# Kernel optimization log

Hardware: AMD Instinct MI355X
Metric: run time of the kernel (lower is better)

Reference implementation:

```python
import jax, jax.numpy as jnp
import numpy as np

HIDDEN = 256
NUM_CLASSES = 25
INPUT_DIM = 76


def _lstm_layer(x, Wi, Wh, b):
    """Flax OptimizedLSTMCell semantics: gates [i, f, g, o], zero-init carry.
    x: [B, T, D]; Wi: [D, 4H]; Wh: [H, 4H]; b: [4H]. Returns hidden seq [B, T, H]."""
    B = x.shape[0]
    H = Wh.shape[0]
    c0 = jnp.zeros((B, H), x.dtype)
    h0 = jnp.zeros((B, H), x.dtype)

    def step(carry, xt):
        c, h = carry
        z = xt @ Wi + h @ Wh + b  # [B, 4H]
        i, f, g, o = jnp.split(z, 4, axis=-1)
        i = jax.nn.sigmoid(i)
        f = jax.nn.sigmoid(f)
        g = jnp.tanh(g)
        o = jax.nn.sigmoid(o)
        c = f * c + i * g
        h = o * jnp.tanh(c)
        return (c, h), h

    (_, _), ys = jax.lax.scan(step, (c0, h0), jnp.swapaxes(x, 0, 1))  # scan over time
    return jnp.swapaxes(ys, 0, 1)  # [B, T, H]


def setup_inputs() -> dict:
    key = jax.random.key(0)
    ks = jax.random.split(key, 9)
    B, T, D, H = 512, 512, INPUT_DIM, HIDDEN
    s_in = 1.0 / np.sqrt(D)
    s_h = 1.0 / np.sqrt(H)
    return {
        "x": jax.random.normal(ks[0], (B, T, D), jnp.float32),
        "Wi1": jax.random.normal(ks[1], (D, 4 * H), jnp.float32) * s_in,
        "Wh1": jax.random.normal(ks[2], (H, 4 * H), jnp.float32) * s_h,
        "b1": jnp.zeros((4 * H,), jnp.float32),
        "Wi2": jax.random.normal(ks[3], (H, 4 * H), jnp.float32) * s_h,
        "Wh2": jax.random.normal(ks[4], (H, 4 * H), jnp.float32) * s_h,
        "b2": jnp.zeros((4 * H,), jnp.float32),
        "Wd": jax.random.normal(ks[5], (H, NUM_CLASSES), jnp.float32) * s_h,
        "bd": jnp.zeros((NUM_CLASSES,), jnp.float32),
    }


def reference(x, Wi1, Wh1, b1, Wi2, Wh2, b2, Wd, bd):
    h1 = _lstm_layer(x, Wi1, Wh1, b1)   # [B, T, H]
    h2 = _lstm_layer(h1, Wi2, Wh2, b2)  # [B, T, H]
    feats = h2[:, -1]                   # dropout deterministic (eval mode)
    logits = feats @ Wd + bd            # [B, num_classes]
    return logits
```

## Files before the change

kernel.cpp:

```cpp
#include <hip/hip_runtime.h>

#define BB 512
#define TT 512
#define DD 76
#define HH 256
#define NC 25
#define NBLK 256
#define NTHREADS 512
#define BBHH (BB * HH)

#define K1 352
#define K2 512
#define WS1 360
#define WS2 520

typedef unsigned short u16;
typedef unsigned int u32;
typedef unsigned long long u64;
typedef __attribute__((ext_vector_type(8))) short bf16x8;
typedef __attribute__((ext_vector_type(4))) float f32x4;

__device__ __forceinline__ float bf2f(u16 v) {
  union { u32 u; float f; } c; c.u = ((u32)v) << 16; return c.f;
}
__device__ __forceinline__ u16 f2bf(float f) {
  union { u32 u; float f; } c; c.f = f;
  u32 r = c.u + 0x7FFFu + ((c.u >> 16) & 1u);
  return (u16)(r >> 16);
}
__device__ __forceinline__ void split2(float f, u16& h, u16& l) {
  u16 hh = f2bf(f);
  float r = f - bf2f(hh);
  h = hh; l = f2bf(r);
}
__device__ __forceinline__ float tanh_f(float v) {
  float e = __expf(2.0f * v);
  return 1.0f - 2.0f / (e + 1.0f);
}
__device__ __forceinline__ float gact(float v, bool is_tanh) {
  float e = __expf(is_tanh ? 2.0f * v : -v);
  float inv = 1.0f / (1.0f + e);
  return is_tanh ? 1.0f - 2.0f * inv : inv;
}

__device__ __forceinline__ u64 ald2(const u32* p) {
  return __hip_atomic_load((const u64*)p, __ATOMIC_RELAXED, __HIP_MEMORY_SCOPE_AGENT);
}
__device__ __forceinline__ u32 ald1(const u32* p) {
  return __hip_atomic_load(p, __ATOMIC_RELAXED, __HIP_MEMORY_SCOPE_AGENT);
}
__device__ __forceinline__ void ast1(u32* p, u32 v) {
  __hip_atomic_store(p, v, __ATOMIC_RELAXED, __HIP_MEMORY_SCOPE_AGENT);
}

__device__ __forceinline__ void wait_flags(const u32* fbase, u32 target) {
  const int tid = threadIdx.x;
  if (tid < 32) {
    const u32* p = fbase + tid * 32;
    while (__hip_atomic_load(p, __ATOMIC_RELAXED, __HIP_MEMORY_SCOPE_AGENT) < target)
      __builtin_amdgcn_s_sleep(1);
  }
  __syncthreads();
}
__device__ __forceinline__ void post_flag(u32* slot, u32 val) {
  __syncthreads();
  if (threadIdx.x == 0) ast1(slot, val);
}

__device__ __forceinline__ bf16x8 hi8(const u64 w[4]) {
  union { u32 u[4]; bf16x8 v; } c;
#pragma unroll
  for (int i = 0; i < 4; ++i)
    c.u[i] = __builtin_amdgcn_perm((u32)(w[i] >> 32), (u32)w[i], 0x05040100u);
  return c.v;
}
__device__ __forceinline__ bf16x8 lo8(const u64 w[4]) {
  union { u32 u[4]; bf16x8 v; } c;
#pragma unroll
  for (int i = 0; i < 4; ++i)
    c.u[i] = __builtin_amdgcn_perm((u32)(w[i] >> 32), (u32)w[i], 0x07060302u);
  return c.v;
}

__device__ __forceinline__ void splitv8(const float* f, bf16x8& vh, bf16x8& vl) {
  union { u16 s[8]; bf16x8 v; } ch, cl;
#pragma unroll
  for (int i = 0; i < 8; ++i) { u16 h_, l_; split2(f[i], h_, l_); ch.s[i] = h_; cl.s[i] = l_; }
  vh = ch.v; vl = cl.v;
}

__global__ void repack_kernel(const float* __restrict__ Wi1, const float* __restrict__ Wh1,
                              const float* __restrict__ Wi2, const float* __restrict__ Wh2,
                              u16* __restrict__ w1hg, u16* __restrict__ w1lg,
                              u16* __restrict__ w2hg, u16* __restrict__ w2lg) {
  int idx = blockIdx.x * blockDim.x + threadIdx.x;
  const int N1 = 1024 * K1;
  if (idx < N1) {
    int c = idx / K1, k = idx - c * K1;
    int src = (c & 3) * HH + (c >> 2);
    float v = 0.f;
    if (k < HH) v = Wh1[k * 1024 + src];
    else if (k < HH + DD) v = Wi1[(k - HH) * 1024 + src];
    u16 h, l; split2(v, h, l);
    w1hg[idx] = h; w1lg[idx] = l;
  } else if (idx < N1 + 1024 * K2) {
    int d = idx - N1;
    int c = d >> 9, k = d & 511;
    int src = (c & 3) * HH + (c >> 2);
    float v = (k < HH) ? Wi2[k * 1024 + src] : Wh2[(k - HH) * 1024 + src];
    u16 h, l; split2(v, h, l);
    w2hg[d] = h; w2lg[d] = l;
  }
}

#define MFMA3(AA, AB, AC, AH, AL, BH, BL)                                   \
  { (AA) = __builtin_amdgcn_mfma_f32_16x16x32_bf16(AH, BH, (AA), 0, 0, 0);  \
    (AB) = __builtin_amdgcn_mfma_f32_16x16x32_bf16(AH, BL, (AB), 0, 0, 0);  \
    (AC) = __builtin_amdgcn_mfma_f32_16x16x32_bf16(AL, BH, (AC), 0, 0, 0); }

#define MFMA_CH(AH, AL, PH0, PL0, PH1, PL1, KOFF)                           \
  { bf16x8 b0h_ = *(const bf16x8*)((PH0) + (KOFF));                         \
    bf16x8 b0l_ = *(const bf16x8*)((PL0) + (KOFF));                         \
    bf16x8 b1h_ = *(const bf16x8*)((PH1) + (KOFF));                         \
    bf16x8 b1l_ = *(const bf16x8*)((PL1) + (KOFF));                         \
    MFMA3(aA0, aB0, aC0, AH, AL, b0h_, b0l_)                                \
    MFMA3(aA1, aB1, aC1, AH, AL, b1h_, b1l_) }

#define GATES(Z, CS, DW)                                                    \
  _Pragma("unroll")                                                         \
  for (int r = 0; r < 4; ++r) {                                             \
    float a_ = gact((Z)[r], gi == 2);                                       \
    float v1_ = __shfl_xor(a_, 1);                                          \
    float v2_ = __shfl_xor(a_, 2);                                          \
    float v3_ = __shfl_xor(a_, 3);                                          \
    float cn_ = v1_ * (CS)[r] + a_ * v2_;                                   \
    (CS)[r] = cn_;                                                          \
    float hv_ = v3_ * tanh_f(cn_);                                          \
    if (gi == 0) {                                                          \
      u16 hh_, hl_; split2(hv_, hh_, hl_);                                  \
      ast1((DW) + (size_t)(rbase + r) * HH + jg, (u32)hh_ | ((u32)hl_ << 16)); \
    }                                                                       \
  }

__global__ __launch_bounds__(NTHREADS, 2) void lstm_kernel(
    const float* __restrict__ x,
    const float* __restrict__ b1, const float* __restrict__ b2,
    const float* __restrict__ Wd, const float* __restrict__ bd,
    const u16* __restrict__ w1hg, const u16* __restrict__ w1lg,
    const u16* __restrict__ w2hg, const u16* __restrict__ w2lg,
    u32* __restrict__ h1w, u32* __restrict__ h2w,
    u32* __restrict__ flags,
    float* __restrict__ out)
{
  __shared__ u16 w1h[32 * WS1], w1l[32 * WS1];
  __shared__ u16 w2h[32 * WS2], w2l[32 * WS2];
  __shared__ float zx[2][8][64][4];

  const int tid = threadIdx.x;
  const int lane = tid & 63;
  const int wv = tid >> 6;
  const int m  = wv & 3;
  const int kh = wv >> 2;
  const int nl = lane & 15;
  const int qd = lane >> 4;
  const int bt = blockIdx.x & 7;
  const int jt = blockIdx.x >> 3;
  const int row0 = bt * 64;

  u32* gAp = flags + bt * 1024;
  u32* gBp = flags + 8192 + bt * 1024;
  u32* gAslot = gAp + jt * 32;
  u32* gBslot = gBp + jt * 32;

  for (int i = tid; i < 32 * (K1 / 2); i += NTHREADS) {
    int c = i / 176, kk = i - c * 176;
    ((u32*)&w1h[c * WS1])[kk] = ((const u32*)(w1hg + (size_t)(jt * 32 + c) * K1))[kk];
    ((u32*)&w1l[c * WS1])[kk] = ((const u32*)(w1lg + (size_t)(jt * 32 + c) * K1))[kk];
  }
  for (int i = tid; i < 32 * (K2 / 2); i += NTHREADS) {
    int c = i >> 8, kk = i & 255;
    ((u32*)&w2h[c * WS2])[kk] = ((const u32*)(w2hg + (size_t)(jt * 32 + c) * K2))[kk];
    ((u32*)&w2l[c * WS2])[kk] = ((const u32*)(w2lg + (size_t)(jt * 32 + c) * K2))[kk];
  }

  const int cg_col = jt * 32 + kh * 16 + nl;
  const int jg = cg_col >> 2;
  const int gi = cg_col & 3;
  const int rbase = row0 + m * 16 + qd * 4;

  float ab1[2], ab2[2];
#pragma unroll
  for (int tl = 0; tl < 2; ++tl) {
    int col = jt * 32 + tl * 16 + nl;
    float v1 = b1[(col & 3) * HH + (col >> 2)];
    float v2 = b2[(col & 3) * HH + (col >> 2)];
    ab1[tl] = (kh == 0) ? v1 : 0.f;
    ab2[tl] = (kh == 0) ? v2 : 0.f;
  }

  const int arow = row0 + m * 16 + nl;

  const u16* pB1h0 = w1h + nl * WS1;
  const u16* pB1l0 = w1l + nl * WS1;
  const u16* pB1h1 = w1h + (16 + nl) * WS1;
  const u16* pB1l1 = w1l + (16 + nl) * WS1;
  const u16* pB2h0 = w2h + nl * WS2;
  const u16* pB2l0 = w2l + nl * WS2;
  const u16* pB2h1 = w2h + (16 + nl) * WS2;
  const u16* pB2l1 = w2l + (16 + nl) * WS2;

  float cs1[4] = {0.f, 0.f, 0.f, 0.f}, cs2[4] = {0.f, 0.f, 0.f, 0.f};
  bf16x8 h1fh[4], h1fl[4];

  __syncthreads();

  {
    f32x4 aA0 = {ab1[0], ab1[0], ab1[0], ab1[0]};
    f32x4 aA1 = {ab1[1], ab1[1], ab1[1], ab1[1]};
    f32x4 aB0 = {0,0,0,0}, aB1 = {0,0,0,0}, aC0 = {0,0,0,0}, aC1 = {0,0,0,0};
    const float* xrow = x + (size_t)arow * TT * DD;
    if (kh == 0) {
#pragma unroll
      for (int ci = 0; ci < 2; ++ci) {
        float xv[8];
        float4 f0 = *(const float4*)(xrow + ci * 32 + qd * 8);
        float4 f1 = *(const float4*)(xrow + ci * 32 + qd * 8 + 4);
        xv[0]=f0.x; xv[1]=f0.y; xv[2]=f0.z; xv[3]=f0.w;
        xv[4]=f1.x; xv[5]=f1.y; xv[6]=f1.z; xv[7]=f1.w;
        bf16x8 xh, xl; splitv8(xv, xh, xl);
        const int koff = (8 + ci) * 32 + qd * 8;
        MFMA_CH(xh, xl, pB1h0, pB1l0, pB1h1, pB1l1, koff)
      }
    } else {
      float xv[8] = {0,0,0,0,0,0,0,0};
      if (qd == 0) {
        float4 f0 = *(const float4*)(xrow + 64);
        float4 f1 = *(const float4*)(xrow + 68);
        xv[0]=f0.x; xv[1]=f0.y; xv[2]=f0.z; xv[3]=f0.w;
        xv[4]=f1.x; xv[5]=f1.y; xv[6]=f1.z; xv[7]=f1.w;
      } else if (qd == 1) {
        float4 f0 = *(const float4*)(xrow + 72);
        xv[0]=f0.x; xv[1]=f0.y; xv[2]=f0.z; xv[3]=f0.w;
      }
      bf16x8 xh, xl; splitv8(xv, xh, xl);
      const int koff = 10 * 32 + qd * 8;
      MFMA_CH(xh, xl, pB1h0, pB1l0, pB1h1, pB1l1, koff)
    }
    f32x4 zk = (kh == 0) ? (aA0 + aB0 + aC0) : (aA1 + aB1 + aC1);
    f32x4 zo = (kh == 0) ? (aA1 + aB1 + aC1) : (aA0 + aB0 + aC0);
    *(f32x4*)&zx[1][wv][lane][0] = zo;
    __syncthreads();
    zk += *(const f32x4*)&zx[1][wv ^ 4][lane][0];
    GATES(zk, cs1, h1w)
    __syncthreads();
    if (tid == 0) { ast1(gAslot, 1u); ast1(gBslot, 1u); }
  }

#pragma unroll 1
  for (int t = 0; t < TT; ++t) {
    const u32* h1cw = h1w + (t & 1) * BBHH;
    u32* h1nw = h1w + ((t + 1) & 1) * BBHH;
    const u32* h2pw = h2w + ((t + 1) & 1) * BBHH;
    u32* h2cw = h2w + (t & 1) * BBHH;

    {
      f32x4 aA0 = {ab2[0], ab2[0], ab2[0], ab2[0]};
      f32x4 aA1 = {ab2[1], ab2[1], ab2[1], ab2[1]};
      f32x4 aB0 = {0,0,0,0}, aB1 = {0,0,0,0}, aC0 = {0,0,0,0}, aC1 = {0,0,0,0};

      wait_flags(gAp, t + 1);
      u64 rw2[4][4];
      if (t > 0) {
        const u32* hp = h2pw + (size_t)arow * HH + kh * 128;
#pragma unroll
        for (int i = 0; i < 4; ++i) {
          const u32* p = hp + i * 32 + qd * 8;
          rw2[i][0] = ald2(p);     rw2[i][1] = ald2(p + 2);
          rw2[i][2] = ald2(p + 4); rw2[i][3] = ald2(p + 6);
        }
      }
      wait_flags(gBp, t + 1);
      u64 rw1[4][4];
      {
        const u32* hp = h1cw + (size_t)arow * HH + kh * 128;
#pragma unroll
        for (int i = 0; i < 4; ++i) {
          const u32* p = hp + i * 32 + qd * 8;
          rw1[i][0] = ald2(p);     rw1[i][1] = ald2(p + 2);
          rw1[i][2] = ald2(p + 4); rw1[i][3] = ald2(p + 6);
        }
      }
      if (t > 0) {
#pragma unroll
        for (int i = 0; i < 4; ++i) {
          bf16x8 ah = hi8(rw2[i]), al = lo8(rw2[i]);
          const int koff = (8 + kh * 4 + i) * 32 + qd * 8;
          MFMA_CH(ah, al, pB2h0, pB2l0, pB2h1, pB2l1, koff)
        }
      }
#pragma unroll
      for (int i = 0; i < 4; ++i) {
        h1fh[i] = hi8(rw1[i]); h1fl[i] = lo8(rw1[i]);
        const int koff = (kh * 4 + i) * 32 + qd * 8;
        MFMA_CH(h1fh[i], h1fl[i], pB2h0, pB2l0, pB2h1, pB2l1, koff)
      }
      f32x4 zk = (kh == 0) ? (aA0 + aB0 + aC0) : (aA1 + aB1 + aC1);
      f32x4 zo = (kh == 0) ? (aA1 + aB1 + aC1) : (aA0 + aB0 + aC0);
      *(f32x4*)&zx[0][wv][lane][0] = zo;
      __syncthreads();
      zk += *(const f32x4*)&zx[0][wv ^ 4][lane][0];
      GATES(zk, cs2, h2cw)
      post_flag(gAslot, t + 2);
    }

    if (t < TT - 1) {
      f32x4 aA0 = {ab1[0], ab1[0], ab1[0], ab1[0]};
      f32x4 aA1 = {ab1[1], ab1[1], ab1[1], ab1[1]};
      f32x4 aB0 = {0,0,0,0}, aB1 = {0,0,0,0}, aC0 = {0,0,0,0}, aC1 = {0,0,0,0};
      const float* xrow = x + ((size_t)arow * TT + (t + 1)) * DD;

      if (kh == 0) {
#pragma unroll
        for (int ci = 0; ci < 2; ++ci) {
          float xv[8];
          float4 f0 = *(const float4*)(xrow + ci * 32 + qd * 8);
          float4 f1 = *(const float4*)(xrow + ci * 32 + qd * 8 + 4);
          xv[0]=f0.x; xv[1]=f0.y; xv[2]=f0.z; xv[3]=f0.w;
          xv[4]=f1.x; xv[5]=f1.y; xv[6]=f1.z; xv[7]=f1.w;
          bf16x8 xh, xl; splitv8(xv, xh, xl);
          const int koff = (8 + ci) * 32 + qd * 8;
          MFMA_CH(xh, xl, pB1h0, pB1l0, pB1h1, pB1l1, koff)
        }
      } else {
        float xv[8] = {0,0,0,0,0,0,0,0};
        if (qd == 0) {
          float4 f0 = *(const float4*)(xrow + 64);
          float4 f1 = *(const float4*)(xrow + 68);
          xv[0]=f0.x; xv[1]=f0.y; xv[2]=f0.z; xv[3]=f0.w;
          xv[4]=f1.x; xv[5]=f1.y; xv[6]=f1.z; xv[7]=f1.w;
        } else if (qd == 1) {
          float4 f0 = *(const float4*)(xrow + 72);
          xv[0]=f0.x; xv[1]=f0.y; xv[2]=f0.z; xv[3]=f0.w;
        }
        bf16x8 xh, xl; splitv8(xv, xh, xl);
        const int koff = 10 * 32 + qd * 8;
        MFMA_CH(xh, xl, pB1h0, pB1l0, pB1h1, pB1l1, koff)
      }
#pragma unroll
      for (int i = 0; i < 4; ++i) {
        const int koff = (kh * 4 + i) * 32 + qd * 8;
        MFMA_CH(h1fh[i], h1fl[i], pB1h0, pB1l0, pB1h1, pB1l1, koff)
      }
      f32x4 zk = (kh == 0) ? (aA0 + aB0 + aC0) : (aA1 + aB1 + aC1);
      f32x4 zo = (kh == 0) ? (aA1 + aB1 + aC1) : (aA0 + aB0 + aC0);
      *(f32x4*)&zx[1][wv][lane][0] = zo;
      __syncthreads();
      zk += *(const f32x4*)&zx[1][wv ^ 4][lane][0];
      GATES(zk, cs1, h1nw)
      post_flag(gBslot, t + 2);
    }
  }

  wait_flags(gAp, TT + 1);
  if (tid < 2 * NC) {
    int r = row0 + jt * 2 + tid / NC;
    int n = tid - (tid / NC) * NC;
    float s = bd[n];
    const u32* fw = h2w + BBHH + (size_t)r * HH;
#pragma unroll 8
    for (int k = 0; k < HH; ++k) {
      u32 w = ald1(fw + k);
      s += (bf2f((u16)w) + bf2f((u16)(w >> 16))) * Wd[k * NC + n];
    }
    out[r * NC + n] = s;
  }
}

extern "C" void kernel_launch(void* const* d_in, const int* in_sizes, int n_in,
                              void* d_out, int out_size, void* d_ws, size_t ws_size,
                              hipStream_t stream) {
  const float* x   = (const float*)d_in[0];
  const float* Wi1 = (const float*)d_in[1];
  const float* Wh1 = (const float*)d_in[2];
  const float* b1  = (const float*)d_in[3];
  const float* Wi2 = (const float*)d_in[4];
  const float* Wh2 = (const float*)d_in[5];
  const float* b2  = (const float*)d_in[6];
  const float* Wd  = (const float*)d_in[7];
  const float* bd  = (const float*)d_in[8];

  char* ws = (char*)d_ws;
  u32* h1w = (u32*)(ws);
  u32* h2w = (u32*)(ws + 1048576u);
  u16* w1hg = (u16*)(ws + 2097152u);
  u16* w1lg = (u16*)(ws + 2097152u + 720896u);
  u16* w2hg = (u16*)(ws + 2097152u + 2u * 720896u);
  u16* w2lg = (u16*)(ws + 2097152u + 2u * 720896u + 1048576u);
  u32* flags = (u32*)(ws + 5636096u);
  float* out = (float*)d_out;

  hipMemsetAsync((void*)flags, 0, 65536, stream);
  const int total = 1024 * K1 + 1024 * K2;
  repack_kernel<<<(total + 255) / 256, 256, 0, stream>>>(
      Wi1, Wh1, Wi2, Wh2, w1hg, w1lg, w2hg, w2lg);

  void* args[] = {
    (void*)&x, (void*)&b1, (void*)&b2, (void*)&Wd, (void*)&bd,
    (void*)&w1hg, (void*)&w1lg, (void*)&w2hg, (void*)&w2lg,
    (void*)&h1w, (void*)&h2w,
    (void*)&flags, (void*)&out
  };
  (void)hipLaunchCooperativeKernel((void*)lstm_kernel, dim3(NBLK),
                                   dim3(NTHREADS), args, 0, stream);
}
```

Measured before the change: 5.749 ms.

## Reorder layer-1 step ahead of layer-2 and coalesce hidden-state stores

Each timestep now computes the layer-1 update for t+1 first, using h1 values prefetched in the previous iteration. The layer-2 step then runs, and the wait and load of the next h1 is placed inside it, so the cross-block flag wait overlaps with layer-2 MFMA work. Hidden-state writes are gathered across lanes with shuffles and issued as two 64-bit stores per row from one lane, instead of scattered 32-bit stores from a quarter of the lanes. The x loads are hoisted ahead of the recurrent MFMAs to hide their latency. The cost is extra register pressure from the prefetched h1 buffer and a reworked synchronization order that must still be correct.

```diff
diff --git a/kernel.cpp b/kernel.cpp
--- a/kernel.cpp
+++ b/kernel.cpp
@@ -50,6 +50,9 @@
   return __hip_atomic_load(p, __ATOMIC_RELAXED, __HIP_MEMORY_SCOPE_AGENT);
 }
 __device__ __forceinline__ void ast1(u32* p, u32 v) {
+  __hip_atomic_store(p, v, __ATOMIC_RELAXED, __HIP_MEMORY_SCOPE_AGENT);
+}
+__device__ __forceinline__ void ast2(u64* p, u64 v) {
   __hip_atomic_store(p, v, __ATOMIC_RELAXED, __HIP_MEMORY_SCOPE_AGENT);
 }
 
@@ -126,21 +129,42 @@
     MFMA3(aA0, aB0, aC0, AH, AL, b0h_, b0l_)                                \
     MFMA3(aA1, aB1, aC1, AH, AL, b1h_, b1l_) }
 
-#define GATES(Z, CS, DW)                                                    \
-  _Pragma("unroll")                                                         \
-  for (int r = 0; r < 4; ++r) {                                             \
-    float a_ = gact((Z)[r], gi == 2);                                       \
-    float v1_ = __shfl_xor(a_, 1);                                          \
-    float v2_ = __shfl_xor(a_, 2);                                          \
-    float v3_ = __shfl_xor(a_, 3);                                          \
-    float cn_ = v1_ * (CS)[r] + a_ * v2_;                                   \
-    (CS)[r] = cn_;                                                          \
-    float hv_ = v3_ * tanh_f(cn_);                                          \
-    if (gi == 0) {                                                          \
+#define GATES_ST(Z, CS, DST)                                                \
+  { u32 hwv[4];                                                             \
+    _Pragma("unroll")                                                       \
+    for (int r = 0; r < 4; ++r) {                                           \
+      float a_ = gact((Z)[r], gi == 2);                                     \
+      float v1_ = __shfl_xor(a_, 1);                                        \
+      float v2_ = __shfl_xor(a_, 2);                                        \
+      float v3_ = __shfl_xor(a_, 3);                                        \
+      float cn_ = v1_ * (CS)[r] + a_ * v2_;                                 \
+      (CS)[r] = cn_;                                                        \
+      float hv_ = v3_ * tanh_f(cn_);                                        \
       u16 hh_, hl_; split2(hv_, hh_, hl_);                                  \
-      ast1((DW) + (size_t)(rbase + r) * HH + jg, (u32)hh_ | ((u32)hl_ << 16)); \
+      hwv[r] = (u32)hh_ | ((u32)hl_ << 16);                                 \
     }                                                                       \
-  }
+    _Pragma("unroll")                                                       \
+    for (int r = 0; r < 4; ++r) {                                           \
+      int base_ = lane & 48;                                                \
+      u32 w1_ = __shfl(hwv[r], base_ + 4);                                  \
+      u32 w2_ = __shfl(hwv[r], base_ + 8);                                  \
+      u32 w3_ = __shfl(hwv[r], base_ + 12);                                 \
+      if (nl == 0) {                                                        \
+        u64* dp_ = (u64*)((DST) + (size_t)(rbase + r) * HH + jt * 8 + kh * 4); \
+        ast2(dp_,     (u64)hwv[r] | ((u64)w1_ << 32));                      \
+        ast2(dp_ + 1, (u64)w2_    | ((u64)w3_ << 32));                      \
+      }                                                                     \
+    }                                                                       \
+  }
+
+#define LOAD_RW(RW, BASEPTR)                                                \
+  { const u32* hp_ = (BASEPTR) + (size_t)arow * HH + kh * 128;              \
+    _Pragma("unroll")                                                       \
+    for (int i_ = 0; i_ < 4; ++i_) {                                        \
+      const u32* p_ = hp_ + i_ * 32 + qd * 8;                               \
+      (RW)[i_][0] = ald2(p_);     (RW)[i_][1] = ald2(p_ + 2);               \
+      (RW)[i_][2] = ald2(p_ + 4); (RW)[i_][3] = ald2(p_ + 6);               \
+    } }
 
 __global__ __launch_bounds__(NTHREADS, 2) void lstm_kernel(
     const float* __restrict__ x,
@@ -184,7 +208,6 @@
   }
 
   const int cg_col = jt * 32 + kh * 16 + nl;
-  const int jg = cg_col >> 2;
   const int gi = cg_col & 3;
   const int rbase = row0 + m * 16 + qd * 4;
 
@@ -210,6 +233,7 @@
   const u16* pB2l1 = w2l + (16 + nl) * WS2;
 
   float cs1[4] = {0.f, 0.f, 0.f, 0.f}, cs2[4] = {0.f, 0.f, 0.f, 0.f};
+  u64 rwh1[4][4];
   bf16x8 h1fh[4], h1fl[4];
 
   __syncthreads();
@@ -251,17 +275,74 @@
     *(f32x4*)&zx[1][wv][lane][0] = zo;
     __syncthreads();
     zk += *(const f32x4*)&zx[1][wv ^ 4][lane][0];
-    GATES(zk, cs1, h1w)
+    GATES_ST(zk, cs1, h1w)
     __syncthreads();
     if (tid == 0) { ast1(gAslot, 1u); ast1(gBslot, 1u); }
+    wait_flags(gBp, 1);
+    LOAD_RW(rwh1, h1w)
   }
 
 #pragma unroll 1
   for (int t = 0; t < TT; ++t) {
-    const u32* h1cw = h1w + (t & 1) * BBHH;
     u32* h1nw = h1w + ((t + 1) & 1) * BBHH;
     const u32* h2pw = h2w + ((t + 1) & 1) * BBHH;
     u32* h2cw = h2w + (t & 1) * BBHH;
+
+#pragma unroll
+    for (int i = 0; i < 4; ++i) { h1fh[i] = hi8(rwh1[i]); h1fl[i] = lo8(rwh1[i]); }
+
+    if (t < TT - 1) {
+      f32x4 aA0 = {ab1[0], ab1[0], ab1[0], ab1[0]};
+      f32x4 aA1 = {ab1[1], ab1[1], ab1[1], ab1[1]};
+      f32x4 aB0 = {0,0,0,0}, aB1 = {0,0,0,0}, aC0 = {0,0,0,0}, aC1 = {0,0,0,0};
+      const float* xrow = x + ((size_t)arow * TT + (t + 1)) * DD;
+
+      float4 xf0, xf1, xf2, xf3;
+      if (kh == 0) {
+        xf0 = *(const float4*)(xrow + qd * 8);
+        xf1 = *(const float4*)(xrow + qd * 8 + 4);
+        xf2 = *(const float4*)(xrow + 32 + qd * 8);
+        xf3 = *(const float4*)(xrow + 32 + qd * 8 + 4);
+      } else {
+        xf0 = make_float4(0,0,0,0); xf1 = make_float4(0,0,0,0);
+        if (qd == 0) {
+          xf0 = *(const float4*)(xrow + 64);
+          xf1 = *(const float4*)(xrow + 68);
+        } else if (qd == 1) {
+          xf0 = *(const float4*)(xrow + 72);
+        }
+      }
+
+#pragma unroll
+      for (int i = 0; i < 4; ++i) {
+        const int koff = (kh * 4 + i) * 32 + qd * 8;
+        MFMA_CH(h1fh[i], h1fl[i], pB1h0, pB1l0, pB1h1, pB1l1, koff)
+      }
+      if (kh == 0) {
+        float xv[8];
+        xv[0]=xf0.x; xv[1]=xf0.y; xv[2]=xf0.z; xv[3]=xf0.w;
+        xv[4]=xf1.x; xv[5]=xf1.y; xv[6]=xf1.z; xv[7]=xf1.w;
+        bf16x8 xh, xl; splitv8(xv, xh, xl);
+        MFMA_CH(xh, xl, pB1h0, pB1l0, pB1h1, pB1l1, 8 * 32 + qd * 8)
+        xv[0]=xf2.x; xv[1]=xf2.y; xv[2]=xf2.z; xv[3]=xf2.w;
+        xv[4]=xf3.x; xv[5]=xf3.y; xv[6]=xf3.z; xv[7]=xf3.w;
+        splitv8(xv, xh, xl);
+        MFMA_CH(xh, xl, pB1h0, pB1l0, pB1h1, pB1l1, 9 * 32 + qd * 8)
+      } else {
+        float xv[8];
+        xv[0]=xf0.x; xv[1]=xf0.y; xv[2]=xf0.z; xv[3]=xf0.w;
+        xv[4]=xf1.x; xv[5]=xf1.y; xv[6]=xf1.z; xv[7]=xf1.w;
+        bf16x8 xh, xl; splitv8(xv, xh, xl);
+        MFMA_CH(xh, xl, pB1h0, pB1l0, pB1h1, pB1l1, 10 * 32 + qd * 8)
+      }
+      f32x4 zk = (kh == 0) ? (aA0 + aB0 + aC0) : (aA1 + aB1 + aC1);
+      f32x4 zo = (kh == 0) ? (aA1 + aB1 + aC1) : (aA0 + aB0 + aC0);
+      *(f32x4*)&zx[1][wv][lane][0] = zo;
+      __syncthreads();
+      zk += *(const f32x4*)&zx[1][wv ^ 4][lane][0];
+      GATES_ST(zk, cs1, h1nw)
+      post_flag(gBslot, t + 2);
+    }
 
     {
       f32x4 aA0 = {ab2[0], ab2[0], ab2[0], ab2[0]};
@@ -269,28 +350,9 @@
       f32x4 aB0 = {0,0,0,0}, aB1 = {0,0,0,0}, aC0 = {0,0,0,0}, aC1 = {0,0,0,0};
 
       wait_flags(gAp, t + 1);
-      u64 rw2[4][4];
       if (t > 0) {
-        const u32* hp = h2pw + (size_t)arow * HH + kh * 128;
-#pragma unroll
-        for (int i = 0; i < 4; ++i) {
-          const u32* p = hp + i * 32 + qd * 8;
-          rw2[i][0] = ald2(p);     rw2[i][1] = ald2(p + 2);
-          rw2[i][2] = ald2(p + 4); rw2[i][3] = ald2(p + 6);
-        }
-      }
-      wait_flags(gBp, t + 1);
-      u64 rw1[4][4];
-      {
-        const u32* hp = h1cw + (size_t)arow * HH + kh * 128;
-#pragma unroll
-        for (int i = 0; i < 4; ++i) {
-          const u32* p = hp + i * 32 + qd * 8;
-          rw1[i][0] = ald2(p);     rw1[i][1] = ald2(p + 2);
-          rw1[i][2] = ald2(p + 4); rw1[i][3] = ald2(p + 6);
-        }
-      }
-      if (t > 0) {
+        u64 rw2[4][4];
+        LOAD_RW(rw2, h2pw)
 #pragma unroll
         for (int i = 0; i < 4; ++i) {
           bf16x8 ah = hi8(rw2[i]), al = lo8(rw2[i]);
@@ -300,64 +362,20 @@
       }
 #pragma unroll
       for (int i = 0; i < 4; ++i) {
-        h1fh[i] = hi8(rw1[i]); h1fl[i] = lo8(rw1[i]);
         const int koff = (kh * 4 + i) * 32 + qd * 8;
         MFMA_CH(h1fh[i], h1fl[i], pB2h0, pB2l0, pB2h1, pB2l1, koff)
+      }
+      if (t < TT - 1) {
+        wait_flags(gBp, t + 2);
+        LOAD_RW(rwh1, h1nw)
       }
       f32x4 zk = (kh == 0) ? (aA0 + aB0 + aC0) : (aA1 + aB1 + aC1);
       f32x4 zo = (kh == 0) ? (aA1 + aB1 + aC1) : (aA0 + aB0 + aC0);
       *(f32x4*)&zx[0][wv][lane][0] = zo;
       __syncthreads();
       zk += *(const f32x4*)&zx[0][wv ^ 4][lane][0];
-      GATES(zk, cs2, h2cw)
+      GATES_ST(zk, cs2, h2cw)
       post_flag(gAslot, t + 2);
-    }
-
-    if (t < TT - 1) {
-      f32x4 aA0 = {ab1[0], ab1[0], ab1[0], ab1[0]};
-      f32x4 aA1 = {ab1[1], ab1[1], ab1[1], ab1[1]};
-      f32x4 aB0 = {0,0,0,0}, aB1 = {0,0,0,0}, aC0 = {0,0,0,0}, aC1 = {0,0,0,0};
-      const float* xrow = x + ((size_t)arow * TT + (t + 1)) * DD;
-
-      if (kh == 0) {
-#pragma unroll
-        for (int ci = 0; ci < 2; ++ci) {
-          float xv[8];
-          float4 f0 = *(const float4*)(xrow + ci * 32 + qd * 8);
-          float4 f1 = *(const float4*)(xrow + ci * 32 + qd * 8 + 4);
-          xv[0]=f0.x; xv[1]=f0.y; xv[2]=f0.z; xv[3]=f0.w;
-          xv[4]=f1.x; xv[5]=f1.y; xv[6]=f1.z; xv[7]=f1.w;
-          bf16x8 xh, xl; splitv8(xv, xh, xl);
-          const int koff = (8 + ci) * 32 + qd * 8;
-          MFMA_CH(xh, xl, pB1h0, pB1l0, pB1h1, pB1l1, koff)
-        }
-      } else {
-        float xv[8] = {0,0,0,0,0,0,0,0};
-        if (qd == 0) {
-          float4 f0 = *(const float4*)(xrow + 64);
-          float4 f1 = *(const float4*)(xrow + 68);
-          xv[0]=f0.x; xv[1]=f0.y; xv[2]=f0.z; xv[3]=f0.w;
-          xv[4]=f1.x; xv[5]=f1.y; xv[6]=f1.z; xv[7]=f1.w;
-        } else if (qd == 1) {
-          float4 f0 = *(const float4*)(xrow + 72);
-          xv[0]=f0.x; xv[1]=f0.y; xv[2]=f0.z; xv[3]=f0.w;
-        }
-        bf16x8 xh, xl; splitv8(xv, xh, xl);
-        const int koff = 10 * 32 + qd * 8;
-        MFMA_CH(xh, xl, pB1h0, pB1l0, pB1h1, pB1l1, koff)
-      }
-#pragma unroll
-      for (int i = 0; i < 4; ++i) {
-        const int koff = (kh * 4 + i) * 32 + qd * 8;
-        MFMA_CH(h1fh[i], h1fl[i], pB1h0, pB1l0, pB1h1, pB1l1, koff)
-      }
-      f32x4 zk = (kh == 0) ? (aA0 + aB0 + aC0) : (aA1 + aB1 + aC1);
-      f32x4 zo = (kh == 0) ? (aA1 + aB1 + aC1) : (aA0 + aB0 + aC0);
-      *(f32x4*)&zx[1][wv][lane][0] = zo;
-      __syncthreads();
-      zk += *(const f32x4*)&zx[1][wv ^ 4][lane][0];
-      GATES(zk, cs1, h1nw)
-      post_flag(gBslot, t + 2);
     }
   }
 
```

New measurement: 5.653 ms. No clear change (-1.7%).
